# Optimization experiments

Hardware: AMD Instinct MI355X
Metric: run time of the kernel (lower is better)

The kernel has to match this reference:

```python
import jax, jax.numpy as jnp
import numpy as np

INPUT_SIZE = 40960
HIDDEN_SIZE = 128
OUTPUT_SIZE = 1
BATCH = 4096


def setup_inputs() -> dict:
    key = jax.random.key(0)
    k1, k2, k3, kw1, kw2, kw3 = jax.random.split(key, 6)
    x1 = jax.random.uniform(k1, (BATCH, INPUT_SIZE), dtype=jnp.float32)
    x2 = jax.random.uniform(k2, (BATCH, INPUT_SIZE), dtype=jnp.float32)
    turn = jax.random.randint(k3, (BATCH,), 0, 2, dtype=jnp.int32)
    # nn.Linear weights: [out_features, in_features], kaiming-uniform-ish scale
    s1 = 1.0 / np.sqrt(INPUT_SIZE)
    s2 = 1.0 / np.sqrt(2 * HIDDEN_SIZE)
    w_us = jax.random.uniform(kw1, (HIDDEN_SIZE, INPUT_SIZE), minval=-s1, maxval=s1, dtype=jnp.float32)
    w_them = jax.random.uniform(kw2, (HIDDEN_SIZE, INPUT_SIZE), minval=-s1, maxval=s1, dtype=jnp.float32)
    w2 = jax.random.uniform(kw3, (OUTPUT_SIZE, 2 * HIDDEN_SIZE), minval=-s2, maxval=s2, dtype=jnp.float32)
    return {"x1": x1, "x2": x2, "turn": turn, "w_us": w_us, "w_them": w_them, "w2": w2}


def reference(x1, x2, turn, w_us, w_them, w2):
    # acc1 = relu(fc1_us(x1)); acc2 = relu(fc1_them(x2))
    acc1 = jax.nn.relu(jnp.einsum('bi,hi->bh', x1, w_us))   # [B, H]
    acc2 = jax.nn.relu(jnp.einsum('bi,hi->bh', x2, w_them)) # [B, H]
    x = jnp.concatenate((acc1, acc2), axis=1)               # [B, 2H]
    return jnp.einsum('bh,oh->bo', x, w2)                   # [B, 1]
```

## Files before the change

kernel.cpp:

```cpp
#include <hip/hip_runtime.h>

#define B_ROWS 4096
#define K_DIM  40960
#define H_DIM  128
#define BM     64
#define BK     64
#define KSPLIT 4
#define KCHUNK (K_DIM / KSPLIT)
#define NT     (KCHUNK / BK)
#define MT     (B_ROWS / BM)

typedef __attribute__((ext_vector_type(4))) float f32x4;
typedef __attribute__((ext_vector_type(8))) short short8;

static_assert(KSPLIT * KCHUNK == K_DIM, "ksplit");
static_assert((NT & 1) == 0, "NT even");

__device__ float g_acc[2u * B_ROWS * H_DIM];

__device__ __forceinline__ unsigned pkbf(float a, float b) {
  unsigned ua = __float_as_uint(a), ub = __float_as_uint(b);
  ua = (ua + 0x7fffu + ((ua >> 16) & 1u)) >> 16;
  ub = (ub + 0x7fffu + ((ub >> 16) & 1u)) & 0xffff0000u;
  return ua | ub;
}

template <bool ATOMIC>
__global__ __launch_bounds__(512, 4) void nnue_stage1(
    const float* __restrict__ x1, const float* __restrict__ x2,
    const float* __restrict__ wus, const float* __restrict__ wthem,
    float* __restrict__ part) {
  __shared__ ushort ldsA[2][BM][BK];
  __shared__ ushort ldsB[2][H_DIM][BK];

  const int t = threadIdx.x;

  const int bid = blockIdx.x;
  const int g   = bid & 7;
  const int mt  = bid >> 3;
  const int mat = g & 1;
  const int ks  = g >> 1;

  const float* __restrict__ X = mat ? x2 : x1;
  const float* __restrict__ W = mat ? wthem : wus;
  const size_t kb0 = (size_t)ks * KCHUNK;

  const int r0 = t >> 4;
  const int c0 = (t & 15) * 4;

  const float* gA0 = X + (size_t)(mt * BM + r0) * K_DIM + kb0 + c0;
  const float* gA1 = gA0 + (size_t)32 * K_DIM;
  const float* gB0 = W + (size_t)r0 * K_DIM + kb0 + c0;

  const int wb0 =
      r0 * 128 + (((((t & 15) >> 1)) ^ (r0 & 7)) << 4) + ((t & 1) * 8);

  const int l   = t & 63;
  const int w   = t >> 6;
  const int wr  = w >> 2;
  const int wc  = w & 3;
  const int fr  = l & 15;
  const int lhi = l >> 4;

  int offA[2], offB[2];
  #pragma unroll
  for (int i = 0; i < 2; ++i) {
    const int ra = wr * 32 + i * 16 + fr;
    offA[i] = ra * 128 + ((lhi ^ (ra & 7)) << 4);
  }
  #pragma unroll
  for (int j = 0; j < 2; ++j) {
    const int cb = wc * 32 + j * 16 + fr;
    offB[j] = cb * 128 + ((lhi ^ (cb & 7)) << 4);
  }

  f32x4 acc[2][2] = {};
  f32x4 s0[6], s1[6];

#define ISSUE(S_, kt_)                                                      \
  do {                                                                      \
    const size_t ko = (size_t)(kt_)*BK;                                     \
    S_[0] = __builtin_nontemporal_load((const f32x4*)(gA0 + ko));           \
    S_[1] = __builtin_nontemporal_load((const f32x4*)(gA1 + ko));           \
    S_[2] = *(const f32x4*)(gB0 + ko);                                      \
    S_[3] = *(const f32x4*)(gB0 + ko + (size_t)32 * K_DIM);                 \
    S_[4] = *(const f32x4*)(gB0 + ko + (size_t)64 * K_DIM);                 \
    S_[5] = *(const f32x4*)(gB0 + ko + (size_t)96 * K_DIM);                 \
  } while (0)

#define PK2(v_) \
  { pkbf((v_)[0], (v_)[1]), pkbf((v_)[2], (v_)[3]) }

#define STAGE(S_, buf_)                                                     \
  do {                                                                      \
    char* bA = (char*)ldsA + (buf_)*8192 + wb0;                             \
    char* bB = (char*)ldsB + (buf_)*16384 + wb0;                            \
    uint2 u0 = PK2(S_[0]); *(uint2*)(bA) = u0;                              \
    uint2 u1 = PK2(S_[1]); *(uint2*)(bA + 4096) = u1;                       \
    uint2 u2 = PK2(S_[2]); *(uint2*)(bB) = u2;                              \
    uint2 u3 = PK2(S_[3]); *(uint2*)(bB + 4096) = u3;                       \
    uint2 u4 = PK2(S_[4]); *(uint2*)(bB + 8192) = u4;                       \
    uint2 u5 = PK2(S_[5]); *(uint2*)(bB + 12288) = u5;                      \
  } while (0)

#define COMPUTE(buf_)                                                       \
  do {                                                                      \
    const char* bA = (const char*)ldsA + (buf_)*8192;                       \
    const char* bB = (const char*)ldsB + (buf_)*16384;                      \
    _Pragma("unroll") for (int kb = 0; kb < 2; ++kb) {                      \
      const int kx = kb * 64;                                               \
      short8 af[2], bg[2];                                                  \
      _Pragma("unroll") for (int i = 0; i < 2; ++i)                         \
          af[i] = *(const short8*)(bA + (offA[i] ^ kx));                    \
      _Pragma("unroll") for (int j = 0; j < 2; ++j)                         \
          bg[j] = *(const short8*)(bB + (offB[j] ^ kx));                    \
      _Pragma("unroll") for (int i = 0; i < 2; ++i)                         \
          _Pragma("unroll") for (int j = 0; j < 2; ++j)                     \
              acc[i][j] = __builtin_amdgcn_mfma_f32_16x16x32_bf16(          \
                  af[i], bg[j], acc[i][j], 0, 0, 0);                        \
    }                                                                       \
  } while (0)

  ISSUE(s0, 0);
  ISSUE(s1, 1);

  for (int kt = 0; kt < NT - 2; kt += 2) {
    STAGE(s0, 0);
    __syncthreads();
    ISSUE(s0, kt + 2);
    COMPUTE(0);
    STAGE(s1, 1);
    __syncthreads();
    ISSUE(s1, kt + 3);
    COMPUTE(1);
  }
  STAGE(s0, 0);
  __syncthreads();
  COMPUTE(0);
  STAGE(s1, 1);
  __syncthreads();
  COMPUTE(1);

#undef ISSUE
#undef PK2
#undef STAGE
#undef COMPUTE

  if (!ATOMIC) {
    float* dst = part + (((size_t)mat * KSPLIT + ks) * B_ROWS) * (size_t)H_DIM;
    #pragma unroll
    for (int i = 0; i < 2; ++i)
      #pragma unroll
      for (int j = 0; j < 2; ++j)
        #pragma unroll
        for (int r = 0; r < 4; ++r) {
          const int rowg = mt * BM + wr * 32 + i * 16 + (lhi << 2) + r;
          const int colg = wc * 32 + j * 16 + fr;
          __builtin_nontemporal_store(acc[i][j][r],
                                      &dst[(size_t)rowg * H_DIM + colg]);
        }
  } else {
    float* dst = g_acc + (size_t)mat * B_ROWS * H_DIM;
    #pragma unroll
    for (int i = 0; i < 2; ++i)
      #pragma unroll
      for (int j = 0; j < 2; ++j)
        #pragma unroll
        for (int r = 0; r < 4; ++r) {
          const int rowg = mt * BM + wr * 32 + i * 16 + (lhi << 2) + r;
          const int colg = wc * 32 + j * 16 + fr;
          atomicAdd(&dst[(size_t)rowg * H_DIM + colg], acc[i][j][r]);
        }
  }
}

__global__ void nnue_zero_acc() {
  const unsigned i = blockIdx.x * 256 + threadIdx.x;
  if (i < 2u * B_ROWS * H_DIM) g_acc[i] = 0.f;
}

template <int KS>
__global__ __launch_bounds__(512) void nnue_stage2(
    const float* __restrict__ part, const float* __restrict__ w2,
    float* __restrict__ out) {
  const float* p = part ? part : (const float*)g_acc;
  const int t = threadIdx.x;
  const int l = t & 63, w = t >> 6;
  const int b = blockIdx.x * 8 + w;
  float a0 = 0.f, a1 = 0.f, a2 = 0.f, a3 = 0.f;
  #pragma unroll
  for (int ks = 0; ks < KS; ++ks) {
    const float* p0 = p + ((size_t)ks * B_ROWS + b) * H_DIM;
    const float* p1 = p + (((size_t)KS + ks) * B_ROWS + b) * H_DIM;
    a0 += __builtin_nontemporal_load(&p0[l]);
    a1 += __builtin_nontemporal_load(&p0[l + 64]);
    a2 += __builtin_nontemporal_load(&p1[l]);
    a3 += __builtin_nontemporal_load(&p1[l + 64]);
  }
  float sv = fmaxf(a0, 0.f) * w2[l] + fmaxf(a1, 0.f) * w2[l + 64] +
             fmaxf(a2, 0.f) * w2[l + 128] + fmaxf(a3, 0.f) * w2[l + 192];
  #pragma unroll
  for (int off = 32; off; off >>= 1) sv += __shfl_xor(sv, off, 64);
  if (l == 0) out[b] = sv;
}

extern "C" void kernel_launch(void* const* d_in, const int* in_sizes, int n_in,
                              void* d_out, int out_size, void* d_ws,
                              size_t ws_size, hipStream_t stream) {
  const float* x1    = (const float*)d_in[0];
  const float* x2    = (const float*)d_in[1];
  const float* wus   = (const float*)d_in[3];
  const float* wthem = (const float*)d_in[4];
  const float* w2    = (const float*)d_in[5];
  float* out = (float*)d_out;

  const size_t PART_BYTES =
      2ull * KSPLIT * B_ROWS * H_DIM * sizeof(float);

  if (ws_size >= PART_BYTES) {
    float* part = (float*)d_ws;
    nnue_stage1<false><<<MT * KSPLIT * 2, 512, 0, stream>>>(x1, x2, wus, wthem,
                                                            part);
    nnue_stage2<KSPLIT><<<B_ROWS / 8, 512, 0, stream>>>(part, w2, out);
  } else {
    nnue_zero_acc<<<(2 * B_ROWS * H_DIM + 255) / 256, 256, 0, stream>>>();
    nnue_stage1<true><<<MT * KSPLIT * 2, 512, 0, stream>>>(x1, x2, wus, wthem,
                                                           nullptr);
    nnue_stage2<1><<<B_ROWS / 8, 512, 0, stream>>>(nullptr, w2, out);
  }
}
```

Measured before the change: 317.4 us.

## Double M tile to 128, split K eight ways, and remap blocks to XCDs

Raises the row tile from 64 to 128 so each staged weight tile is reused across twice as many batch rows. This halves the redundant fp32 weight traffic and bf16 conversion per MFMA. K is split eight ways instead of four, which keeps the same block count (512) for occupancy. Block IDs are remapped so that blocks sharing a weight K-slice land on the same XCD, for L2 reuse. The weight tile is now single-buffered in registers and the A tile double-buffered, which raises register pressure and doubles the partial-sum traffic that stage 2 must read.

```diff
diff --git a/kernel.cpp b/kernel.cpp
--- a/kernel.cpp
+++ b/kernel.cpp
@@ -3,9 +3,9 @@
 #define B_ROWS 4096
 #define K_DIM  40960
 #define H_DIM  128
-#define BM     64
+#define BM     128
 #define BK     64
-#define KSPLIT 4
+#define KSPLIT 8
 #define KCHUNK (K_DIM / KSPLIT)
 #define NT     (KCHUNK / BK)
 #define MT     (B_ROWS / BM)
@@ -35,11 +35,13 @@
 
   const int t = threadIdx.x;
 
-  const int bid = blockIdx.x;
-  const int g   = bid & 7;
-  const int mt  = bid >> 3;
-  const int mat = g & 1;
-  const int ks  = g >> 1;
+  const int bid  = blockIdx.x;
+  const int xcd  = bid & 7;
+  const int slot = bid >> 3;
+  const int g    = xcd + 8 * (slot >> 5);
+  const int mt   = slot & 31;
+  const int mat  = g & 1;
+  const int ks   = g >> 1;
 
   const float* __restrict__ X = mat ? x2 : x1;
   const float* __restrict__ W = mat ? wthem : wus;
@@ -48,12 +50,11 @@
   const int r0 = t >> 4;
   const int c0 = (t & 15) * 4;
 
-  const float* gA0 = X + (size_t)(mt * BM + r0) * K_DIM + kb0 + c0;
-  const float* gA1 = gA0 + (size_t)32 * K_DIM;
-  const float* gB0 = W + (size_t)r0 * K_DIM + kb0 + c0;
+  const float* gA = X + (size_t)(mt * BM + r0) * K_DIM + kb0 + c0;
+  const float* gB = W + (size_t)r0 * K_DIM + kb0 + c0;
 
   const int wb0 =
-      r0 * 128 + (((((t & 15) >> 1)) ^ (r0 & 7)) << 4) + ((t & 1) * 8);
+      r0 * 128 + ((((t & 15) >> 1) ^ (r0 & 7)) << 4) + ((t & 1) * 8);
 
   const int l   = t & 63;
   const int w   = t >> 6;
@@ -62,10 +63,10 @@
   const int fr  = l & 15;
   const int lhi = l >> 4;
 
-  int offA[2], offB[2];
-  #pragma unroll
-  for (int i = 0; i < 2; ++i) {
-    const int ra = wr * 32 + i * 16 + fr;
+  int offA[4], offB[2];
+  #pragma unroll
+  for (int i = 0; i < 4; ++i) {
+    const int ra = wr * 64 + i * 16 + fr;
     offA[i] = ra * 128 + ((lhi ^ (ra & 7)) << 4);
   }
   #pragma unroll
@@ -74,87 +75,100 @@
     offB[j] = cb * 128 + ((lhi ^ (cb & 7)) << 4);
   }
 
-  f32x4 acc[2][2] = {};
-  f32x4 s0[6], s1[6];
-
-#define ISSUE(S_, kt_)                                                      \
-  do {                                                                      \
-    const size_t ko = (size_t)(kt_)*BK;                                     \
-    S_[0] = __builtin_nontemporal_load((const f32x4*)(gA0 + ko));           \
-    S_[1] = __builtin_nontemporal_load((const f32x4*)(gA1 + ko));           \
-    S_[2] = *(const f32x4*)(gB0 + ko);                                      \
-    S_[3] = *(const f32x4*)(gB0 + ko + (size_t)32 * K_DIM);                 \
-    S_[4] = *(const f32x4*)(gB0 + ko + (size_t)64 * K_DIM);                 \
-    S_[5] = *(const f32x4*)(gB0 + ko + (size_t)96 * K_DIM);                 \
-  } while (0)
-
-#define PK2(v_) \
-  { pkbf((v_)[0], (v_)[1]), pkbf((v_)[2], (v_)[3]) }
-
-#define STAGE(S_, buf_)                                                     \
-  do {                                                                      \
-    char* bA = (char*)ldsA + (buf_)*8192 + wb0;                             \
+  f32x4 acc[4][2] = {};
+  f32x4 sA0[4], sA1[4], sB[4];
+
+#define ISSUE_A(S_, kt_)                                                    \
+  do {                                                                      \
+    const float* pa = gA + (size_t)(kt_)*BK;                                \
+    _Pragma("unroll") for (int r = 0; r < 4; ++r)                           \
+        S_[r] = __builtin_nontemporal_load(                                 \
+            (const f32x4*)(pa + (size_t)r * 32 * K_DIM));                   \
+  } while (0)
+
+#define ISSUE_B(kt_)                                                        \
+  do {                                                                      \
+    const float* pb = gB + (size_t)(kt_)*BK;                                \
+    _Pragma("unroll") for (int r = 0; r < 4; ++r)                           \
+        sB[r] = *(const f32x4*)(pb + (size_t)r * 32 * K_DIM);               \
+  } while (0)
+
+#define STAGE_A(S_, buf_)                                                   \
+  do {                                                                      \
+    char* bA = (char*)ldsA + (buf_)*16384 + wb0;                            \
+    _Pragma("unroll") for (int r = 0; r < 4; ++r) {                         \
+      uint2 u;                                                              \
+      u.x = pkbf(S_[r][0], S_[r][1]);                                       \
+      u.y = pkbf(S_[r][2], S_[r][3]);                                       \
+      *(uint2*)(bA + r * 4096) = u;                                         \
+    }                                                                       \
+  } while (0)
+
+#define STAGE_B(buf_)                                                       \
+  do {                                                                      \
     char* bB = (char*)ldsB + (buf_)*16384 + wb0;                            \
-    uint2 u0 = PK2(S_[0]); *(uint2*)(bA) = u0;                              \
-    uint2 u1 = PK2(S_[1]); *(uint2*)(bA + 4096) = u1;                       \
-    uint2 u2 = PK2(S_[2]); *(uint2*)(bB) = u2;                              \
-    uint2 u3 = PK2(S_[3]); *(uint2*)(bB + 4096) = u3;                       \
-    uint2 u4 = PK2(S_[4]); *(uint2*)(bB + 8192) = u4;                       \
-    uint2 u5 = PK2(S_[5]); *(uint2*)(bB + 12288) = u5;                      \
+    _Pragma("unroll") for (int r = 0; r < 4; ++r) {                         \
+      uint2 u;                                                              \
+      u.x = pkbf(sB[r][0], sB[r][1]);                                       \
+      u.y = pkbf(sB[r][2], sB[r][3]);                                       \
+      *(uint2*)(bB + r * 4096) = u;                                         \
+    }                                                                       \
   } while (0)
 
 #define COMPUTE(buf_)                                                       \
   do {                                                                      \
-    const char* bA = (const char*)ldsA + (buf_)*8192;                       \
+    const char* bA = (const char*)ldsA + (buf_)*16384;                      \
     const char* bB = (const char*)ldsB + (buf_)*16384;                      \
     _Pragma("unroll") for (int kb = 0; kb < 2; ++kb) {                      \
       const int kx = kb * 64;                                               \
-      short8 af[2], bg[2];                                                  \
-      _Pragma("unroll") for (int i = 0; i < 2; ++i)                         \
+      short8 af[4], bg[2];                                                  \
+      _Pragma("unroll") for (int i = 0; i < 4; ++i)                         \
           af[i] = *(const short8*)(bA + (offA[i] ^ kx));                    \
       _Pragma("unroll") for (int j = 0; j < 2; ++j)                         \
           bg[j] = *(const short8*)(bB + (offB[j] ^ kx));                    \
-      _Pragma("unroll") for (int i = 0; i < 2; ++i)                         \
+      _Pragma("unroll") for (int i = 0; i < 4; ++i)                         \
           _Pragma("unroll") for (int j = 0; j < 2; ++j)                     \
               acc[i][j] = __builtin_amdgcn_mfma_f32_16x16x32_bf16(          \
                   af[i], bg[j], acc[i][j], 0, 0, 0);                        \
     }                                                                       \
   } while (0)
 
-  ISSUE(s0, 0);
-  ISSUE(s1, 1);
-
-  for (int kt = 0; kt < NT - 2; kt += 2) {
-    STAGE(s0, 0);
+  ISSUE_A(sA0, 0);
+  ISSUE_A(sA1, 1);
+  ISSUE_B(0);
+
+  for (int kt = 0; kt < NT; kt += 2) {
+    STAGE_A(sA0, 0);
+    STAGE_B(0);
     __syncthreads();
-    ISSUE(s0, kt + 2);
+    ISSUE_B(kt + 1);
+    if (kt + 2 < NT) ISSUE_A(sA0, kt + 2);
     COMPUTE(0);
-    STAGE(s1, 1);
+    STAGE_A(sA1, 1);
+    STAGE_B(1);
     __syncthreads();
-    ISSUE(s1, kt + 3);
+    if (kt + 2 < NT) {
+      ISSUE_B(kt + 2);
+      if (kt + 3 < NT) ISSUE_A(sA1, kt + 3);
+    }
     COMPUTE(1);
   }
-  STAGE(s0, 0);
-  __syncthreads();
-  COMPUTE(0);
-  STAGE(s1, 1);
-  __syncthreads();
-  COMPUTE(1);
-
-#undef ISSUE
-#undef PK2
-#undef STAGE
+
+#undef ISSUE_A
+#undef ISSUE_B
+#undef STAGE_A
+#undef STAGE_B
 #undef COMPUTE
 
   if (!ATOMIC) {
     float* dst = part + (((size_t)mat * KSPLIT + ks) * B_ROWS) * (size_t)H_DIM;
     #pragma unroll
-    for (int i = 0; i < 2; ++i)
+    for (int i = 0; i < 4; ++i)
       #pragma unroll
       for (int j = 0; j < 2; ++j)
         #pragma unroll
         for (int r = 0; r < 4; ++r) {
-          const int rowg = mt * BM + wr * 32 + i * 16 + (lhi << 2) + r;
+          const int rowg = mt * BM + wr * 64 + i * 16 + (lhi << 2) + r;
           const int colg = wc * 32 + j * 16 + fr;
           __builtin_nontemporal_store(acc[i][j][r],
                                       &dst[(size_t)rowg * H_DIM + colg]);
@@ -162,12 +176,12 @@
   } else {
     float* dst = g_acc + (size_t)mat * B_ROWS * H_DIM;
     #pragma unroll
-    for (int i = 0; i < 2; ++i)
+    for (int i = 0; i < 4; ++i)
       #pragma unroll
       for (int j = 0; j < 2; ++j)
         #pragma unroll
         for (int r = 0; r < 4; ++r) {
-          const int rowg = mt * BM + wr * 32 + i * 16 + (lhi << 2) + r;
+          const int rowg = mt * BM + wr * 64 + i * 16 + (lhi << 2) + r;
           const int colg = wc * 32 + j * 16 + fr;
           atomicAdd(&dst[(size_t)rowg * H_DIM + colg], acc[i][j][r]);
         }
```

Measured after the change: 276.9 us (median of 2 runs). 1.15x faster.
